# Optimization experiments

Measured on AMD Instinct MI355X. Metric: run time of the kernel, lower is better.

Reference implementation:

```python
import jax, jax.numpy as jnp
import numpy as np

INPUT_DIM = 1024
HIDDEN_DIM = 64   # per-head dim
NUM_HEADS = 16
PROJ = HIDDEN_DIM * NUM_HEADS  # 1024


def setup_inputs() -> dict:
    key = jax.random.key(0)
    ks = jax.random.split(key, 9)
    s = 1.0 / np.sqrt(INPUT_DIM)
    x = jax.random.normal(ks[0], (4, 2048, INPUT_DIM), dtype=jnp.float32)
    # Linear weights stored [in, out] (math-equivalent to torch's W.T)
    Wq = jax.random.uniform(ks[1], (INPUT_DIM, PROJ), jnp.float32, -s, s)
    bq = jax.random.uniform(ks[2], (PROJ,), jnp.float32, -s, s)
    Wk = jax.random.uniform(ks[3], (INPUT_DIM, PROJ), jnp.float32, -s, s)
    bk = jax.random.uniform(ks[4], (PROJ,), jnp.float32, -s, s)
    Wv = jax.random.uniform(ks[5], (INPUT_DIM, PROJ), jnp.float32, -s, s)
    bv = jax.random.uniform(ks[6], (PROJ,), jnp.float32, -s, s)
    sf = 1.0 / np.sqrt(PROJ)
    Wf = jax.random.uniform(ks[7], (PROJ, HIDDEN_DIM), jnp.float32, -sf, sf)
    bf = jax.random.uniform(ks[8], (HIDDEN_DIM,), jnp.float32, -sf, sf)
    return {"x": x, "Wq": Wq, "bq": bq, "Wk": Wk, "bk": bk,
            "Wv": Wv, "bv": bv, "Wf": Wf, "bf": bf}


def reference(x, Wq, bq, Wk, bk, Wv, bv, Wf, bf):
    B, S, _ = x.shape
    def split_heads(t):  # [B,S,H*D] -> [B,H,S,D]
        return t.reshape(B, S, NUM_HEADS, HIDDEN_DIM).transpose(0, 2, 1, 3)
    q = split_heads(x @ Wq + bq)
    k = split_heads(x @ Wk + bk)
    v = split_heads(x @ Wv + bv)
    scale = 1.0 / jnp.sqrt(jnp.float32(HIDDEN_DIM))
    scores = jnp.einsum('bhqd,bhkd->bhqk', q, k) * scale  # [B,H,S,S]
    weights = jax.nn.softmax(scores, axis=-1)
    ctx = jnp.einsum('bhqk,bhkd->bhqd', weights, v)
    ctx = ctx.transpose(0, 2, 1, 3).reshape(B, S, PROJ)
    return ctx @ Wf + bf  # [B,S,HIDDEN_DIM]
```

## Files before the change

kernel.cpp:

```cpp
#include <hip/hip_runtime.h>
#include <math.h>

#define S_LEN 2048
#define NH 16
#define HD 64
#define DMODEL 1024
#define BATCH 4
#define M_TOT (BATCH * S_LEN)

typedef __attribute__((ext_vector_type(8))) short bf16x8;
typedef __attribute__((ext_vector_type(4))) float f32x4;

#define CK 0.18033688f

__device__ __forceinline__ unsigned short f2bf_rne(float f) {
    unsigned u = __float_as_uint(f);
    u += 0x7fffu + ((u >> 16) & 1u);
    return (unsigned short)(u >> 16);
}

__device__ __forceinline__ void gld16(unsigned short* lds, const unsigned short* g) {
    __builtin_amdgcn_global_load_lds(
        (const __attribute__((address_space(1))) void*)g,
        (__attribute__((address_space(3))) void*)lds, 16, 0, 0);
}

__global__ __launch_bounds__(256) void cvt_fused(
    const float* __restrict__ x,
    const float* __restrict__ Wq, const float* __restrict__ Wk,
    const float* __restrict__ Wv, const float* __restrict__ Wf,
    unsigned short* __restrict__ xb, unsigned short* __restrict__ WT)
{
    const int z = blockIdx.z;
    const int tid = threadIdx.x;

    if (z < 4) {
        if (z == 3 && blockIdx.x > 0) return;
        const float* W = (z == 0) ? Wq : (z == 1) ? Wk : (z == 2) ? Wv : Wf;
        const int ncol = (z == 3) ? 64 : DMODEL;
        unsigned short* out = WT + (size_t)z * DMODEL * DMODEL;

        __shared__ float Lt[64][65];
        const int r0 = blockIdx.y * 64;
        const int c0 = blockIdx.x * 64;

        #pragma unroll
        for (int p = 0; p < 4; p++) {
            int row = (tid >> 4) + p * 16;
            int c4 = (tid & 15) * 4;
            float4 v = *(const float4*)(W + (size_t)(r0 + row) * ncol + c0 + c4);
            Lt[row][c4 + 0] = v.x; Lt[row][c4 + 1] = v.y;
            Lt[row][c4 + 2] = v.z; Lt[row][c4 + 3] = v.w;
        }
        __syncthreads();
        #pragma unroll
        for (int p = 0; p < 4; p++) {
            int nr = (tid >> 4) + p * 16;
            int kc = (tid & 15) * 4;
            unsigned short t[4];
            #pragma unroll
            for (int j = 0; j < 4; j++) t[j] = f2bf_rne(Lt[kc + j][nr]);
            *(uint2*)(out + (size_t)(c0 + nr) * DMODEL + r0 + kc) = *(uint2*)t;
        }
    } else {
        const int gtid = (blockIdx.y * 16 + blockIdx.x) * 256 + tid;
        #pragma unroll
        for (int it = 0; it < 8; it++) {
            #pragma unroll
            for (int k = 0; k < 4; k++) {
                size_t i = ((size_t)((it * 4 + k) * 65536) + gtid) * 4;
                float4 v = *(const float4*)(x + i);
                unsigned short t[4];
                t[0] = f2bf_rne(v.x); t[1] = f2bf_rne(v.y);
                t[2] = f2bf_rne(v.z); t[3] = f2bf_rne(v.w);
                *(uint2*)(xb + i) = *(uint2*)t;
            }
        }
    }
}

__global__ __launch_bounds__(512) void qkv_gemm_mfma(
    const unsigned short* __restrict__ xb,
    const unsigned short* __restrict__ WT,
    const float* __restrict__ bq, const float* __restrict__ bk,
    const float* __restrict__ bv,
    unsigned short* __restrict__ Qb, unsigned short* __restrict__ Kb,
    unsigned short* __restrict__ Vtb)
{
    __shared__ __align__(16) unsigned short As[3][16 * 512];
    __shared__ __align__(16) unsigned short Bs[3][32 * 512];

    const int lin = blockIdx.x;
    const int xcd = lin & 7;
    const int s   = lin >> 3;
    const int rb  = xcd * 4 + (s & 3);
    const int ocz = s >> 2;
    const int ocb = ocz & 7;
    const int z   = ocz >> 3;

    const unsigned short* Wz = WT + (size_t)z * DMODEL * DMODEL;
    const float* bias = (z == 0) ? bq : (z == 1) ? bk : bv;

    const int tid = threadIdx.x;
    const int lane = tid & 63, w = tid >> 6;
    const int quad = lane >> 4, l15 = lane & 15;
    const int wq = w & 1;
    const int wr = w >> 1;

    const int OC0 = ocb * 128;
    const int R0  = rb * 256;

    const unsigned short* gA  = Wz + (size_t)(OC0 + w * 16 + l15) * DMODEL + quad * 8;
    const unsigned short* gB0 = xb + (size_t)(R0  + w * 16 + l15) * DMODEL + quad * 8;
    const unsigned short* gB1 = gB0 + (size_t)128 * DMODEL;

    f32x4 acc[4][4];
    #pragma unroll
    for (int i = 0; i < 4; i++)
        #pragma unroll
        for (int j = 0; j < 4; j++)
            #pragma unroll
            for (int c = 0; c < 4; c++) acc[i][j][c] = 0.f;

#define QKV_STAGE(At, Bt, K)  do {                                 \
        gld16((At) + (w * 2 + 0) * 512, gA  + (K));                \
        gld16((At) + (w * 2 + 1) * 512, gA  + (K) + 32);           \
        gld16((Bt) + (w * 2 + 0) * 512, gB0 + (K));                \
        gld16((Bt) + (w * 2 + 1) * 512, gB0 + (K) + 32);           \
        gld16((Bt) + ((w + 8) * 2 + 0) * 512, gB1 + (K));          \
        gld16((Bt) + ((w + 8) * 2 + 1) * 512, gB1 + (K) + 32);     \
    } while (0)

    QKV_STAGE(As[0], Bs[0], 0);
    QKV_STAGE(As[1], Bs[1], 64);

    int cur = 0;
    for (int t = 0; t < 16; ++t) {
        if (t < 15) asm volatile("s_waitcnt vmcnt(6)" ::: "memory");
        else        asm volatile("s_waitcnt vmcnt(0)" ::: "memory");
        __builtin_amdgcn_s_barrier();

        if (t <= 13) {
            int nb = cur + 2; if (nb >= 3) nb -= 3;
            QKV_STAGE(As[nb], Bs[nb], (t + 2) * 64);
        }

        const unsigned short* Ab = As[cur];
        const unsigned short* Bb = Bs[cur];

        __builtin_amdgcn_s_setprio(1);
        #pragma unroll
        for (int sl = 0; sl < 2; sl++) {
            bf16x8 af[4], bfr[4];
            #pragma unroll
            for (int i = 0; i < 4; i++)
                af[i]  = *(const bf16x8*)&Ab[((wq * 4 + i) * 2 + sl) * 512 + lane * 8];
            #pragma unroll
            for (int j = 0; j < 4; j++)
                bfr[j] = *(const bf16x8*)&Bb[((wr * 4 + j) * 2 + sl) * 512 + lane * 8];
            if (z != 2) {
                #pragma unroll
                for (int i = 0; i < 4; i++)
                    #pragma unroll
                    for (int j = 0; j < 4; j++)
                        acc[i][j] = __builtin_amdgcn_mfma_f32_16x16x32_bf16(
                            af[i], bfr[j], acc[i][j], 0, 0, 0);
            } else {
                #pragma unroll
                for (int i = 0; i < 4; i++)
                    #pragma unroll
                    for (int j = 0; j < 4; j++)
                        acc[i][j] = __builtin_amdgcn_mfma_f32_16x16x32_bf16(
                            bfr[j], af[i], acc[i][j], 0, 0, 0);
            }
        }
        __builtin_amdgcn_s_setprio(0);

        if (++cur == 3) cur = 0;
    }
#undef QKV_STAGE

    if (z != 2) {
        unsigned short* out = (z == 0) ? Qb : Kb;
        const float qs = (z == 0) ? CK : 1.0f;
        #pragma unroll
        for (int i = 0; i < 4; i++) {
            int oc = OC0 + wq * 64 + i * 16 + quad * 4;
            float4 bv4 = *(const float4*)&bias[oc];
            #pragma unroll
            for (int j = 0; j < 4; j++) {
                int row = R0 + wr * 64 + j * 16 + l15;
                unsigned short t4[4];
                t4[0] = f2bf_rne((acc[i][j][0] + bv4.x) * qs);
                t4[1] = f2bf_rne((acc[i][j][1] + bv4.y) * qs);
                t4[2] = f2bf_rne((acc[i][j][2] + bv4.z) * qs);
                t4[3] = f2bf_rne((acc[i][j][3] + bv4.w) * qs);
                *(uint2*)(out + (size_t)row * DMODEL + oc) = *(uint2*)t4;
            }
        }
    } else {
        const int b = R0 >> 11;
        const int sbase = (R0 & 2047) + wr * 64;
        #pragma unroll
        for (int i = 0; i < 4; i++) {
            int oc = OC0 + wq * 64 + i * 16 + l15;
            float bvv = bias[oc];
            #pragma unroll
            for (int j = 0; j < 4; j++) {
                int sq = sbase + j * 16 + quad * 4;
                unsigned short t4[4];
                t4[0] = f2bf_rne(acc[i][j][0] + bvv);
                t4[1] = f2bf_rne(acc[i][j][1] + bvv);
                t4[2] = f2bf_rne(acc[i][j][2] + bvv);
                t4[3] = f2bf_rne(acc[i][j][3] + bvv);
                *(uint2*)(Vtb + (size_t)(b * DMODEL + oc) * S_LEN + sq) = *(uint2*)t4;
            }
        }
    }
}

__global__ __launch_bounds__(256, 4) void flash_attn_mfma(
    const unsigned short* __restrict__ Qg,
    const unsigned short* __restrict__ Kg,
    const unsigned short* __restrict__ Vtg,
    unsigned short* __restrict__ ctxb)
{
    __shared__ __align__(16) unsigned short Ks[16 * 512];
    __shared__ __align__(16) unsigned short Vs[16 * 512];
    __shared__ __align__(16) unsigned short Ps[8 * 512];

    const int tid  = threadIdx.x;
    const int lane = tid & 63, w = tid >> 6;
    const int quad = lane >> 4, l15 = lane & 15;

    const int lin = blockIdx.x + 16 * (blockIdx.y + 16 * blockIdx.z);
    const int xcd = lin & 7;
    const int s   = lin >> 3;
    const int bh  = xcd + 8 * (s >> 4);
    const int qblk = s & 15;
    const int b = bh >> 4, h = bh & 15;
    const int r0 = qblk * 128;

    bf16x8 qf[2][2];
    #pragma unroll
    for (int nt = 0; nt < 2; nt++)
        #pragma unroll
        for (int ds = 0; ds < 2; ds++)
            qf[nt][ds] = *(const bf16x8*)(Qg +
                (size_t)(b * S_LEN + r0 + w * 32 + nt * 16 + l15) * DMODEL +
                h * HD + ds * 32 + quad * 8);

    const unsigned short* gK = Kg + (size_t)(b * S_LEN + w * 16 + l15) * DMODEL + h * HD + quad * 8;
    const unsigned short* gV = Vtg + ((size_t)((b * NH + h) * HD + w * 16 + l15)) * S_LEN + quad * 8;

    f32x4 O[2][4], lsum[2];
    #pragma unroll
    for (int rt = 0; rt < 2; rt++) {
        #pragma unroll
        for (int c = 0; c < 4; c++) lsum[rt][c] = 0.f;
        #pragma unroll
        for (int dt = 0; dt < 4; dt++)
            #pragma unroll
            for (int c = 0; c < 4; c++) O[rt][dt][c] = 0.f;
    }

    f32x4 zero4;
    #pragma unroll
    for (int c = 0; c < 4; c++) zero4[c] = 0.f;
    bf16x8 ones;
    #pragma unroll
    for (int c = 0; c < 8; c++) ones[c] = (short)0x3F80;

    for (int st = 0; st < S_LEN / 128; st++) {
        __syncthreads();
        gld16(Ks + ((w + 0) * 2 + 0) * 512, gK);
        gld16(Ks + ((w + 0) * 2 + 1) * 512, gK + 32);
        gld16(Ks + ((w + 4) * 2 + 0) * 512, gK + (size_t)64 * DMODEL);
        gld16(Ks + ((w + 4) * 2 + 1) * 512, gK + (size_t)64 * DMODEL + 32);
        gld16(Vs + (w * 4 + 0) * 512, gV);
        gld16(Vs + (w * 4 + 1) * 512, gV + 32);
        gld16(Vs + (w * 4 + 2) * 512, gV + 64);
        gld16(Vs + (w * 4 + 3) * 512, gV + 96);
        gK += (size_t)128 * DMODEL;
        gV += 128;
        __syncthreads();

        #pragma unroll
        for (int r = 0; r < 4; r++) {
            f32x4 sc[2][2];
            {
                bf16x8 kf0 = *(const bf16x8*)&Ks[((r * 2 + 0) * 2 + 0) * 512 + lane * 8];
                bf16x8 kf1 = *(const bf16x8*)&Ks[((r * 2 + 1) * 2 + 0) * 512 + lane * 8];
                sc[0][0] = __builtin_amdgcn_mfma_f32_16x16x32_bf16(kf0, qf[0][0], zero4, 0, 0, 0);
                sc[0][1] = __builtin_amdgcn_mfma_f32_16x16x32_bf16(kf0, qf[1][0], zero4, 0, 0, 0);
                sc[1][0] = __builtin_amdgcn_mfma_f32_16x16x32_bf16(kf1, qf[0][0], zero4, 0, 0, 0);
                sc[1][1] = __builtin_amdgcn_mfma_f32_16x16x32_bf16(kf1, qf[1][0], zero4, 0, 0, 0);
                kf0 = *(const bf16x8*)&Ks[((r * 2 + 0) * 2 + 1) * 512 + lane * 8];
                kf1 = *(const bf16x8*)&Ks[((r * 2 + 1) * 2 + 1) * 512 + lane * 8];
                sc[0][0] = __builtin_amdgcn_mfma_f32_16x16x32_bf16(kf0, qf[0][1], sc[0][0], 0, 0, 0);
                sc[0][1] = __builtin_amdgcn_mfma_f32_16x16x32_bf16(kf0, qf[1][1], sc[0][1], 0, 0, 0);
                sc[1][0] = __builtin_amdgcn_mfma_f32_16x16x32_bf16(kf1, qf[0][1], sc[1][0], 0, 0, 0);
                sc[1][1] = __builtin_amdgcn_mfma_f32_16x16x32_bf16(kf1, qf[1][1], sc[1][1], 0, 0, 0);
            }

            #pragma unroll
            for (int nt = 0; nt < 2; nt++) {
                #pragma unroll
                for (int mt = 0; mt < 2; mt++) {
                    unsigned u[4];
                    #pragma unroll
                    for (int c = 0; c < 4; c++)
                        u[c] = __float_as_uint(__builtin_amdgcn_exp2f(sc[mt][nt][c]));
                    uint2 pk;
                    pk.x = __builtin_amdgcn_perm(u[1], u[0], 0x07060302u);
                    pk.y = __builtin_amdgcn_perm(u[3], u[2], 0x07060302u);
                    int off = (w * 2 + nt) * 512 + (mt * 2 + (quad >> 1)) * 128 +
                              l15 * 8 + (quad & 1) * 4;
                    *(uint2*)&Ps[off] = pk;
                }
            }

            bf16x8 pf0 = *(const bf16x8*)&Ps[(w * 2 + 0) * 512 + lane * 8];
            bf16x8 pf1 = *(const bf16x8*)&Ps[(w * 2 + 1) * 512 + lane * 8];
            lsum[0] = __builtin_amdgcn_mfma_f32_16x16x32_bf16(pf0, ones, lsum[0], 0, 0, 0);
            lsum[1] = __builtin_amdgcn_mfma_f32_16x16x32_bf16(pf1, ones, lsum[1], 0, 0, 0);
            #pragma unroll
            for (int dt = 0; dt < 4; dt++) {
                bf16x8 vf = *(const bf16x8*)&Vs[(dt * 4 + r) * 512 + lane * 8];
                O[0][dt] = __builtin_amdgcn_mfma_f32_16x16x32_bf16(pf0, vf, O[0][dt], 0, 0, 0);
                O[1][dt] = __builtin_amdgcn_mfma_f32_16x16x32_bf16(pf1, vf, O[1][dt], 0, 0, 0);
            }
        }
    }

    const size_t srow = (size_t)(b * S_LEN + r0 + w * 32);
    #pragma unroll
    for (int rt = 0; rt < 2; rt++) {
        #pragma unroll
        for (int reg = 0; reg < 4; reg++) {
            float li = 1.0f / lsum[rt][reg];
            size_t rowoff = (srow + rt * 16 + quad * 4 + reg) * DMODEL + h * HD + l15;
            #pragma unroll
            for (int dt = 0; dt < 4; dt++)
                ctxb[rowoff + dt * 16] = f2bf_rne(O[rt][dt][reg] * li);
        }
    }
}

__global__ __launch_bounds__(512) void out_proj_mfma(
    const unsigned short* __restrict__ ctxb,
    const unsigned short* __restrict__ WfT,
    const float* __restrict__ bfb,
    float* __restrict__ out)
{
    __shared__ float Red[8 * 1024];

    const int tid = threadIdx.x;
    const int lane = tid & 63, w = tid >> 6;
    const int quad = lane >> 4, l15 = lane & 15;
    const int m0 = blockIdx.x * 16;

    const unsigned short* pA = ctxb + (size_t)(m0 + l15) * DMODEL + w * 128 + quad * 8;
    const unsigned short* pB = WfT + (size_t)l15 * DMODEL + w * 128 + quad * 8;

    f32x4 acc[4];
    #pragma unroll
    for (int j = 0; j < 4; j++)
        #pragma unroll
        for (int c = 0; c < 4; c++) acc[j][c] = 0.f;

    #pragma unroll
    for (int k0 = 0; k0 < 128; k0 += 32) {
        bf16x8 af = *(const bf16x8*)(pA + k0);
        #pragma unroll
        for (int j = 0; j < 4; j++) {
            bf16x8 bfr = *(const bf16x8*)(pB + (size_t)j * 16 * DMODEL + k0);
            acc[j] = __builtin_amdgcn_mfma_f32_16x16x32_bf16(af, bfr, acc[j], 0, 0, 0);
        }
    }

    #pragma unroll
    for (int j = 0; j < 4; j++)
        #pragma unroll
        for (int reg = 0; reg < 4; reg++)
            Red[w * 1024 + lane * 16 + j * 4 + reg] = acc[j][reg];
    __syncthreads();

    const int row = tid >> 5;
    const int c0  = (tid & 31) * 2;
    float2 o;
    float* op = &o.x;
    #pragma unroll
    for (int cc = 0; cc < 2; cc++) {
        int col = c0 + cc;
        int idx = ((row >> 2) * 16 + (col & 15)) * 16 + (col >> 4) * 4 + (row & 3);
        float s = 0.f;
        #pragma unroll
        for (int wv = 0; wv < 8; wv++) s += Red[wv * 1024 + idx];
        op[cc] = s + bfb[col];
    }
    *(float2*)(out + (size_t)(m0 + row) * HD + c0) = o;
}

extern "C" void kernel_launch(void* const* d_in, const int* in_sizes, int n_in,
                              void* d_out, int out_size, void* d_ws, size_t ws_size,
                              hipStream_t stream)
{
    (void)in_sizes; (void)n_in; (void)out_size; (void)ws_size;
    const float* x  = (const float*)d_in[0];
    const float* Wq = (const float*)d_in[1];
    const float* bq = (const float*)d_in[2];
    const float* Wk = (const float*)d_in[3];
    const float* bk = (const float*)d_in[4];
    const float* Wv = (const float*)d_in[5];
    const float* bv = (const float*)d_in[6];
    const float* Wf = (const float*)d_in[7];
    const float* bf = (const float*)d_in[8];
    float* out = (float*)d_out;

    char* wsb = (char*)d_ws;
    unsigned short* xb   = (unsigned short*)wsb;
    unsigned short* ctxb = (unsigned short*)wsb;
    unsigned short* WT   = xb + (size_t)M_TOT * DMODEL;
    unsigned short* WfT  = WT + (size_t)3 * DMODEL * DMODEL;
    unsigned short* Qb   = (unsigned short*)(wsb + (size_t)32 * 1024 * 1024);
    unsigned short* Kb   = Qb + (size_t)M_TOT * DMODEL;
    unsigned short* Vtb  = Kb + (size_t)M_TOT * DMODEL;

    cvt_fused<<<dim3(16, 16, 5), 256, 0, stream>>>(x, Wq, Wk, Wv, Wf, xb, WT);
    qkv_gemm_mfma<<<dim3(768), 512, 0, stream>>>(xb, WT, bq, bk, bv, Qb, Kb, Vtb);
    flash_attn_mfma<<<dim3(S_LEN / 128, NH, BATCH), 256, 0, stream>>>(Qb, Kb, Vtb, ctxb);
    out_proj_mfma<<<dim3(M_TOT / 16), 512, 0, stream>>>(ctxb, WfT, bf, out);
}
```

Measured before the change: 293.0 us.

## Fuse Q/K/V projections into one tile sharing each x tile across three weights

Each QKV GEMM block now computes a 256-row by 64-column tile for all three of Q, K and V together, so one x tile in LDS feeds three weight tiles instead of being reloaded once per projection. The grid shrinks from 768 to 512 blocks, and each wave now works on 32 rows across three output matrices. The pipeline also drops from triple-buffered loads with vmcnt waits and setprio to plain double buffering with __syncthreads. That gives less load/compute overlap and lower arithmetic intensity per weight tile, and may raise register pressure.

```diff
diff --git a/kernel.cpp b/kernel.cpp
--- a/kernel.cpp
+++ b/kernel.cpp
@@ -79,7 +79,7 @@
     }
 }
 
-__global__ __launch_bounds__(512) void qkv_gemm_mfma(
+__global__ __launch_bounds__(512) void qkv_fused_mfma(
     const unsigned short* __restrict__ xb,
     const unsigned short* __restrict__ WT,
     const float* __restrict__ bq, const float* __restrict__ bk,
@@ -87,132 +87,130 @@
     unsigned short* __restrict__ Qb, unsigned short* __restrict__ Kb,
     unsigned short* __restrict__ Vtb)
 {
-    __shared__ __align__(16) unsigned short As[3][16 * 512];
-    __shared__ __align__(16) unsigned short Bs[3][32 * 512];
+    __shared__ __align__(16) unsigned short Ws[2][24 * 512];
+    __shared__ __align__(16) unsigned short Bs[2][32 * 512];
 
     const int lin = blockIdx.x;
     const int xcd = lin & 7;
     const int s   = lin >> 3;
     const int rb  = xcd * 4 + (s & 3);
-    const int ocz = s >> 2;
-    const int ocb = ocz & 7;
-    const int z   = ocz >> 3;
-
-    const unsigned short* Wz = WT + (size_t)z * DMODEL * DMODEL;
-    const float* bias = (z == 0) ? bq : (z == 1) ? bk : bv;
+    const int ocb = s >> 2;
 
     const int tid = threadIdx.x;
     const int lane = tid & 63, w = tid >> 6;
     const int quad = lane >> 4, l15 = lane & 15;
-    const int wq = w & 1;
-    const int wr = w >> 1;
-
-    const int OC0 = ocb * 128;
+
     const int R0  = rb * 256;
-
-    const unsigned short* gA  = Wz + (size_t)(OC0 + w * 16 + l15) * DMODEL + quad * 8;
-    const unsigned short* gB0 = xb + (size_t)(R0  + w * 16 + l15) * DMODEL + quad * 8;
+    const int OC0 = ocb * 64;
+
+    const unsigned short* gW0 = WT +
+        (size_t)(OC0 + (w >> 1) * 16 + l15) * DMODEL + (w & 1) * 32 + quad * 8;
+    const unsigned short* gW1 = gW0 + (size_t)DMODEL * DMODEL;
+    const unsigned short* gW2 = gW1 + (size_t)DMODEL * DMODEL;
+    const unsigned short* gB0 = xb + (size_t)(R0 + w * 16 + l15) * DMODEL + quad * 8;
     const unsigned short* gB1 = gB0 + (size_t)128 * DMODEL;
 
-    f32x4 acc[4][4];
-    #pragma unroll
-    for (int i = 0; i < 4; i++)
-        #pragma unroll
-        for (int j = 0; j < 4; j++)
-            #pragma unroll
-            for (int c = 0; c < 4; c++) acc[i][j][c] = 0.f;
-
-#define QKV_STAGE(At, Bt, K)  do {                                 \
-        gld16((At) + (w * 2 + 0) * 512, gA  + (K));                \
-        gld16((At) + (w * 2 + 1) * 512, gA  + (K) + 32);           \
-        gld16((Bt) + (w * 2 + 0) * 512, gB0 + (K));                \
-        gld16((Bt) + (w * 2 + 1) * 512, gB0 + (K) + 32);           \
-        gld16((Bt) + ((w + 8) * 2 + 0) * 512, gB1 + (K));          \
-        gld16((Bt) + ((w + 8) * 2 + 1) * 512, gB1 + (K) + 32);     \
+    f32x4 acc[3][4][2];
+    #pragma unroll
+    for (int z = 0; z < 3; z++)
+        #pragma unroll
+        for (int i = 0; i < 4; i++)
+            #pragma unroll
+            for (int j = 0; j < 2; j++)
+                #pragma unroll
+                for (int c = 0; c < 4; c++) acc[z][i][j][c] = 0.f;
+
+#define QKV_STAGE(BUF, K)  do {                                        \
+        gld16(Ws[BUF] + (0 * 8 + w) * 512, gW0 + (K));                 \
+        gld16(Ws[BUF] + (1 * 8 + w) * 512, gW1 + (K));                 \
+        gld16(Ws[BUF] + (2 * 8 + w) * 512, gW2 + (K));                 \
+        gld16(Bs[BUF] + ((w + 0) * 2 + 0) * 512, gB0 + (K));           \
+        gld16(Bs[BUF] + ((w + 0) * 2 + 1) * 512, gB0 + (K) + 32);      \
+        gld16(Bs[BUF] + ((w + 8) * 2 + 0) * 512, gB1 + (K));           \
+        gld16(Bs[BUF] + ((w + 8) * 2 + 1) * 512, gB1 + (K) + 32);      \
     } while (0)
 
-    QKV_STAGE(As[0], Bs[0], 0);
-    QKV_STAGE(As[1], Bs[1], 64);
-
-    int cur = 0;
+    QKV_STAGE(0, 0);
+
     for (int t = 0; t < 16; ++t) {
-        if (t < 15) asm volatile("s_waitcnt vmcnt(6)" ::: "memory");
-        else        asm volatile("s_waitcnt vmcnt(0)" ::: "memory");
-        __builtin_amdgcn_s_barrier();
-
-        if (t <= 13) {
-            int nb = cur + 2; if (nb >= 3) nb -= 3;
-            QKV_STAGE(As[nb], Bs[nb], (t + 2) * 64);
-        }
-
-        const unsigned short* Ab = As[cur];
+        const int cur = t & 1;
+        __syncthreads();
+        if (t < 15) {
+            if (cur == 0) QKV_STAGE(1, (t + 1) * 64);
+            else          QKV_STAGE(0, (t + 1) * 64);
+        }
+
+        const unsigned short* Wb = Ws[cur];
         const unsigned short* Bb = Bs[cur];
 
-        __builtin_amdgcn_s_setprio(1);
         #pragma unroll
         for (int sl = 0; sl < 2; sl++) {
-            bf16x8 af[4], bfr[4];
-            #pragma unroll
-            for (int i = 0; i < 4; i++)
-                af[i]  = *(const bf16x8*)&Ab[((wq * 4 + i) * 2 + sl) * 512 + lane * 8];
-            #pragma unroll
-            for (int j = 0; j < 4; j++)
-                bfr[j] = *(const bf16x8*)&Bb[((wr * 4 + j) * 2 + sl) * 512 + lane * 8];
-            if (z != 2) {
+            bf16x8 bfr[2];
+            #pragma unroll
+            for (int j = 0; j < 2; j++)
+                bfr[j] = *(const bf16x8*)&Bb[((2 * w + j) * 2 + sl) * 512 + lane * 8];
+            #pragma unroll
+            for (int z = 0; z < 3; z++) {
+                bf16x8 af[4];
                 #pragma unroll
                 for (int i = 0; i < 4; i++)
+                    af[i] = *(const bf16x8*)&Wb[(z * 8 + i * 2 + sl) * 512 + lane * 8];
+                if (z != 2) {
                     #pragma unroll
-                    for (int j = 0; j < 4; j++)
-                        acc[i][j] = __builtin_amdgcn_mfma_f32_16x16x32_bf16(
-                            af[i], bfr[j], acc[i][j], 0, 0, 0);
-            } else {
-                #pragma unroll
-                for (int i = 0; i < 4; i++)
+                    for (int i = 0; i < 4; i++)
+                        #pragma unroll
+                        for (int j = 0; j < 2; j++)
+                            acc[z][i][j] = __builtin_amdgcn_mfma_f32_16x16x32_bf16(
+                                af[i], bfr[j], acc[z][i][j], 0, 0, 0);
+                } else {
                     #pragma unroll
-                    for (int j = 0; j < 4; j++)
-                        acc[i][j] = __builtin_amdgcn_mfma_f32_16x16x32_bf16(
-                            bfr[j], af[i], acc[i][j], 0, 0, 0);
-            }
-        }
-        __builtin_amdgcn_s_setprio(0);
-
-        if (++cur == 3) cur = 0;
+                    for (int i = 0; i < 4; i++)
+                        #pragma unroll
+                        for (int j = 0; j < 2; j++)
+                            acc[2][i][j] = __builtin_amdgcn_mfma_f32_16x16x32_bf16(
+                                bfr[j], af[i], acc[2][i][j], 0, 0, 0);
+                }
+            }
+        }
     }
 #undef QKV_STAGE
 
-    if (z != 2) {
+    #pragma unroll
+    for (int z = 0; z < 2; z++) {
         unsigned short* out = (z == 0) ? Qb : Kb;
+        const float* bias = (z == 0) ? bq : bk;
         const float qs = (z == 0) ? CK : 1.0f;
         #pragma unroll
         for (int i = 0; i < 4; i++) {
-            int oc = OC0 + wq * 64 + i * 16 + quad * 4;
+            int oc = OC0 + i * 16 + quad * 4;
             float4 bv4 = *(const float4*)&bias[oc];
             #pragma unroll
-            for (int j = 0; j < 4; j++) {
-                int row = R0 + wr * 64 + j * 16 + l15;
+            for (int j = 0; j < 2; j++) {
+                int row = R0 + w * 32 + j * 16 + l15;
                 unsigned short t4[4];
-                t4[0] = f2bf_rne((acc[i][j][0] + bv4.x) * qs);
-                t4[1] = f2bf_rne((acc[i][j][1] + bv4.y) * qs);
-                t4[2] = f2bf_rne((acc[i][j][2] + bv4.z) * qs);
-                t4[3] = f2bf_rne((acc[i][j][3] + bv4.w) * qs);
+                t4[0] = f2bf_rne((acc[z][i][j][0] + bv4.x) * qs);
+                t4[1] = f2bf_rne((acc[z][i][j][1] + bv4.y) * qs);
+                t4[2] = f2bf_rne((acc[z][i][j][2] + bv4.z) * qs);
+                t4[3] = f2bf_rne((acc[z][i][j][3] + bv4.w) * qs);
                 *(uint2*)(out + (size_t)row * DMODEL + oc) = *(uint2*)t4;
             }
         }
-    } else {
+    }
+    {
         const int b = R0 >> 11;
-        const int sbase = (R0 & 2047) + wr * 64;
+        const int sbase = (R0 & 2047) + w * 32;
         #pragma unroll
         for (int i = 0; i < 4; i++) {
-            int oc = OC0 + wq * 64 + i * 16 + l15;
-            float bvv = bias[oc];
-            #pragma unroll
-            for (int j = 0; j < 4; j++) {
+            int oc = OC0 + i * 16 + l15;
+            float bvv = bv[oc];
+            #pragma unroll
+            for (int j = 0; j < 2; j++) {
                 int sq = sbase + j * 16 + quad * 4;
                 unsigned short t4[4];
-                t4[0] = f2bf_rne(acc[i][j][0] + bvv);
-                t4[1] = f2bf_rne(acc[i][j][1] + bvv);
-                t4[2] = f2bf_rne(acc[i][j][2] + bvv);
-                t4[3] = f2bf_rne(acc[i][j][3] + bvv);
+                t4[0] = f2bf_rne(acc[2][i][j][0] + bvv);
+                t4[1] = f2bf_rne(acc[2][i][j][1] + bvv);
+                t4[2] = f2bf_rne(acc[2][i][j][2] + bvv);
+                t4[3] = f2bf_rne(acc[2][i][j][3] + bvv);
                 *(uint2*)(Vtb + (size_t)(b * DMODEL + oc) * S_LEN + sq) = *(uint2*)t4;
             }
         }
@@ -428,7 +426,7 @@
     unsigned short* Vtb  = Kb + (size_t)M_TOT * DMODEL;
 
     cvt_fused<<<dim3(16, 16, 5), 256, 0, stream>>>(x, Wq, Wk, Wv, Wf, xb, WT);
-    qkv_gemm_mfma<<<dim3(768), 512, 0, stream>>>(xb, WT, bq, bk, bv, Qb, Kb, Vtb);
+    qkv_fused_mfma<<<dim3(512), 512, 0, stream>>>(xb, WT, bq, bk, bv, Qb, Kb, Vtb);
     flash_attn_mfma<<<dim3(S_LEN / 128, NH, BATCH), 256, 0, stream>>>(Qb, Kb, Vtb, ctxb);
     out_proj_mfma<<<dim3(M_TOT / 16), 512, 0, stream>>>(ctxb, WfT, bf, out);
 }
```

After: 268.6 us. -8.3%, faster.
